# Kernel tuning notes

Measured on AMD Instinct MI355X. Metric: run time of the kernel, lower is better.

## Reference

```python
import jax, jax.numpy as jnp
import numpy as np

B, S, D, H = 2, 1024, 1024, 16
DH = D // H            # dim per head = 64
MAX_REL = 32           # max relative positions
ROPE_BASE = 10000.0


def entmax15(X, axis=-1):
    """1.5-entmax with full sort (k=None path of the torch code)."""
    X = (X - jnp.max(X, axis=axis, keepdims=True)) / 2.0
    Xsrt = -jnp.sort(-X, axis=axis)                       # descending sort
    d = X.shape[axis]
    rho = jnp.arange(1, d + 1, dtype=X.dtype)             # broadcasts on last axis
    mean = jnp.cumsum(Xsrt, axis=axis) / rho
    mean_sq = jnp.cumsum(Xsrt * Xsrt, axis=axis) / rho
    ss = rho * (mean_sq - mean * mean)
    delta = (1.0 - ss) / rho
    tau = mean - jnp.sqrt(jnp.clip(delta, 0.0))
    support = jnp.sum(tau <= Xsrt, axis=axis, keepdims=True)
    tau_star = jnp.take_along_axis(tau, support - 1, axis=axis)
    Y = jnp.clip(X - tau_star, 0.0)
    return Y * Y


def _rope(x, cos, sin):
    # x: [B,S,H,DH]; cos/sin: [S, DH//2]; complex mult on (even,odd) pairs
    xe, xo = x[..., 0::2], x[..., 1::2]
    c = cos[None, :, None, :]
    s = sin[None, :, None, :]
    re = xe * c - xo * s
    im = xe * s + xo * c
    return jnp.stack([re, im], axis=-1).reshape(x.shape)


def setup_inputs() -> dict:
    key = jax.random.key(0)
    ks = jax.random.split(key, 10)
    sc = 0.02
    x = jax.random.normal(ks[0], (B, S, D), dtype=jnp.float32)
    w_q = jax.random.normal(ks[1], (D, D), dtype=jnp.float32) * sc
    w_k = jax.random.normal(ks[2], (D, D), dtype=jnp.float32) * sc
    w_v = jax.random.normal(ks[3], (D, D), dtype=jnp.float32) * sc
    w_o = jax.random.normal(ks[4], (D, D), dtype=jnp.float32) * sc
    b_q = jnp.zeros((D,), jnp.float32)
    b_k = jnp.zeros((D,), jnp.float32)
    b_v = jnp.zeros((D,), jnp.float32)
    b_o = jnp.zeros((D,), jnp.float32)
    rel_emb = jax.random.normal(ks[5], (2 * MAX_REL + 1, DH), dtype=jnp.float32) * sc
    inv_freq = 1.0 / (ROPE_BASE ** (np.arange(0, DH, 2, dtype=np.float32) / DH))
    ang = np.arange(S, dtype=np.float32)[:, None] * inv_freq[None, :]
    rope_cos = jnp.asarray(np.cos(ang), jnp.float32)
    rope_sin = jnp.asarray(np.sin(ang), jnp.float32)
    return {"x": x, "w_q": w_q, "b_q": b_q, "w_k": w_k, "b_k": b_k,
            "w_v": w_v, "b_v": b_v, "w_o": w_o, "b_o": b_o,
            "rel_emb": rel_emb, "rope_cos": rope_cos, "rope_sin": rope_sin}


def reference(x, w_q, b_q, w_k, b_k, w_v, b_v, w_o, b_o, rel_emb, rope_cos, rope_sin):
    # QKV projections -> [B,S,H,DH]
    q = (x @ w_q + b_q).reshape(B, S, H, DH)
    k = (x @ w_k + b_k).reshape(B, S, H, DH)
    v = (x @ w_v + b_v).reshape(B, S, H, DH).transpose(0, 2, 1, 3)  # [B,H,S,DH]
    # RoPE on q, k (applied in [B,S,H,DH] layout like the torch code)
    q = _rope(q, rope_cos, rope_sin).transpose(0, 2, 1, 3)  # [B,H,S,DH]
    k = _rope(k, rope_cos, rope_sin).transpose(0, 2, 1, 3)
    q = q / jnp.sqrt(jnp.asarray(DH, q.dtype))
    # content scores
    scores = jnp.einsum('bhqd,bhkd->bhqk', q, k)
    # relative position bias (Shaw et al.), shared embedding for keys & values
    r = jnp.arange(S)
    dist = jnp.clip(r[None, :] - r[:, None], -MAX_REL, MAX_REL) + MAX_REL  # [S,S]
    rel = rel_emb[dist]                                                   # [S,S,DH]
    scores = scores + jnp.einsum('bhqd,qkd->bhqk', q, rel)
    # sparse normalization
    attn = entmax15(scores, axis=-1)
    # context + relative-position values
    ctx = jnp.einsum('bhqk,bhkd->bhqd', attn, v) + jnp.einsum('bhqk,qkd->bhqd', attn, rel)
    out = ctx.transpose(0, 2, 1, 3).reshape(B, S, D) @ w_o + b_o
    return out
```

## Files before the change

kernel.cpp:

```cpp
#include <hip/hip_runtime.h>

typedef __attribute__((ext_vector_type(8))) short s8v;
typedef __attribute__((ext_vector_type(4))) short s4v;
typedef __attribute__((ext_vector_type(4))) float f4v;

__device__ __forceinline__ short f2bf(float f){
  union { float f; unsigned u; } v; v.f = f;
  unsigned r = v.u + 0x7fffu + ((v.u >> 16) & 1u);
  return (short)(r >> 16);
}
__device__ __forceinline__ float bf2f(short s){
  union { unsigned u; float f; } v; v.u = ((unsigned)(unsigned short)s) << 16; return v.f;
}
__device__ __forceinline__ void gload16(const void* g, void* l){
  __builtin_amdgcn_global_load_lds((const __attribute__((address_space(1))) unsigned int*)g,
                                   (__attribute__((address_space(3))) unsigned int*)l, 16, 0, 0);
}

__global__ __launch_bounds__(256) void prep_k(const float* __restrict__ w_q, const float* __restrict__ w_k,
                                              const float* __restrict__ w_v, const float* __restrict__ w_o,
                                              const float* __restrict__ x, const float* __restrict__ rel,
                                              short* __restrict__ wqkvT, short* __restrict__ woT,
                                              short* __restrict__ xb, short* __restrict__ relb,
                                              short* __restrict__ relT){
  int z = blockIdx.z;
  if (z < 4){
    __shared__ float t[64][65];
    const float* in = (z==0) ? w_q : (z==1) ? w_k : (z==2) ? w_v : w_o;
    short* out = (z==3) ? woT : (wqkvT + ((size_t)z<<20));
    int c0 = blockIdx.x*64, r0 = blockIdx.y*64;
    int tx = threadIdx.x & 63, ty = threadIdx.x >> 6;
    #pragma unroll
    for (int i=0;i<16;i++){ int r = ty + i*4; t[r][tx] = in[(size_t)(r0+r)*1024 + c0+tx]; }
    __syncthreads();
    #pragma unroll
    for (int i=0;i<16;i++){ int cc = ty + i*4; out[(size_t)(c0+cc)*1024 + r0+tx] = f2bf(t[tx][cc]); }
    if (z==3 && blockIdx.x==0 && blockIdx.y==0){
      for (int e = threadIdx.x; e < 65*64; e += 256){
        int j = e >> 6, d = e & 63;
        short bv = f2bf(rel[e]);
        relb[e] = bv;
        relT[d*72 + j] = bv;
      }
    }
  } else {
    int bid = (z-4)*256 + blockIdx.y*16 + blockIdx.x;
    int i = bid*256 + threadIdx.x;
    #pragma unroll
    for (int p=0;p<4;p++){
      int idx = p*131072 + i;
      f4v v = ((const f4v*)x)[idx];
      s4v o; o[0]=f2bf(v[0]); o[1]=f2bf(v[1]); o[2]=f2bf(v[2]); o[3]=f2bf(v[3]);
      ((s4v*)xb)[idx] = o;
    }
  }
}

__device__ __forceinline__ void gemm12864_core(const short* __restrict__ A, const short* __restrict__ Bt,
                                               int m0, int n0, short* As, short* Bs, f4v acc[4][2]){
  int tid = threadIdx.x;
  int lane = tid & 63, wave = tid >> 6;
  int wr = wave >> 1, wc = wave & 1, g = lane >> 4, c = lane & 15;
  int lrow = lane >> 3;
  int scol = ((lane & 7) ^ lrow) * 8;
  for (int k0 = 0; k0 < 1024; k0 += 64){
    #pragma unroll
    for (int p=0;p<4;p++){
      int r0 = wave*32 + p*8;
      gload16(A + (size_t)(m0 + r0 + lrow)*1024 + k0 + scol, &As[r0*64]);
    }
    #pragma unroll
    for (int p=0;p<2;p++){
      int r0 = wave*16 + p*8;
      gload16(Bt + (size_t)(n0 + r0 + lrow)*1024 + k0 + scol, &Bs[r0*64]);
    }
    __syncthreads();
    #pragma unroll
    for (int ks=0;ks<2;ks++){
      s8v a[4], b[2];
      int pu = ((ks*4 + g) ^ (c & 7))*8;
      #pragma unroll
      for (int mi=0;mi<4;mi++) a[mi] = *(const s8v*)(&As[(wr*64 + mi*16 + c)*64 + pu]);
      #pragma unroll
      for (int ni=0;ni<2;ni++) b[ni] = *(const s8v*)(&Bs[(wc*32 + ni*16 + c)*64 + pu]);
      #pragma unroll
      for (int mi=0;mi<4;mi++)
        #pragma unroll
        for (int ni=0;ni<2;ni++)
          acc[mi][ni] = __builtin_amdgcn_mfma_f32_16x16x32_bf16(a[mi], b[ni], acc[mi][ni], 0,0,0);
    }
    __syncthreads();
  }
}

__global__ __launch_bounds__(256) void gemm_qkv_k(const short* __restrict__ A, const short* __restrict__ Bt,
                                                  const float* __restrict__ b_q, const float* __restrict__ b_k,
                                                  const float* __restrict__ b_v,
                                                  const float* __restrict__ cs, const float* __restrict__ sn,
                                                  short* __restrict__ Qb, short* __restrict__ Kb,
                                                  short* __restrict__ Vt){
  __shared__ __align__(16) char lbuf[24576];
  short* As = (short*)lbuf;
  short* Bs = (short*)(lbuf + 16384);
  short* st = (short*)lbuf;
  int flat = blockIdx.x;
  int swz = (flat & 7)*96 + (flat >> 3);
  int m0 = (swz / 48) * 128, n0 = (swz % 48) * 64;
  int lane = threadIdx.x & 63, wave = threadIdx.x >> 6;
  int wr = wave >> 1, wc = wave & 1, g = lane >> 4, c = lane & 15;
  f4v acc[4][2] = {};
  gemm12864_core(A, Bt, m0, n0, As, Bs, acc);

  int sec = n0 >> 10;
  const float* bias = (sec==0) ? b_q : (sec==1) ? b_k : b_v;
  int b = m0 >> 10, s0 = m0 & 1023, h0 = (n0 & 1023) >> 6;
  #pragma unroll
  for (int mi=0;mi<4;mi++)
    #pragma unroll
    for (int ni=0;ni<2;ni++){
      int cl = wc*32 + ni*16 + c;
      float bi = bias[(n0 & 1023) + cl];
      int ifr = cl >> 1;
      #pragma unroll
      for (int i=0;i<4;i++){
        int rl = wr*64 + mi*16 + g*4 + i;
        float v = acc[mi][ni][i] + bi;
        if (sec < 2){
          int s = s0 + rl;
          float co = cs[s*32 + ifr], si = sn[s*32 + ifr];
          float p = __shfl_xor(v, 1, 64);
          float o = (cl & 1) ? fmaf(p, si, v*co) : fmaf(v, co, -(p*si));
          if (sec == 0) o *= 0.125f;
          v = o;
        }
        st[rl*66 + cl] = f2bf(v);
      }
    }
  __syncthreads();
  if (sec < 2){
    short* dst = (sec==0) ? Qb : Kb;
    size_t base = ((size_t)(b*16+h0)*1024 + s0)*64;
    for (int e = threadIdx.x; e < 128*16; e += 256){
      int row = e >> 4, cl4 = (e & 15)*4;
      s4v o = *(const s4v*)(&st[row*66 + cl4]);
      *(s4v*)(&dst[base + (size_t)row*64 + cl4]) = o;
    }
  } else {
    size_t base = (size_t)(b*16+h0)*65536;
    for (int e = threadIdx.x; e < 64*32; e += 256){
      int d = e >> 5, s4 = (e & 31)*4;
      s4v o;
      o[0] = st[(s4+0)*66 + d]; o[1] = st[(s4+1)*66 + d];
      o[2] = st[(s4+2)*66 + d]; o[3] = st[(s4+3)*66 + d];
      *(s4v*)(&Vt[base + (size_t)d*1024 + s0 + s4]) = o;
    }
  }
}

__global__ __launch_bounds__(256) void gemm_out_k(const short* __restrict__ A, const short* __restrict__ Bt,
                                                  const float* __restrict__ bias, float* __restrict__ C){
  __shared__ __align__(16) short As[128*64];
  __shared__ __align__(16) short Bs[64*64];
  int flat = blockIdx.x;
  int swz = (flat & 7)*32 + (flat >> 3);
  int m0 = (swz >> 4)*128, n0 = (swz & 15)*64;
  int lane = threadIdx.x & 63, wave = threadIdx.x >> 6;
  int wr = wave >> 1, wc = wave & 1, g = lane >> 4, c = lane & 15;
  f4v acc[4][2] = {};
  gemm12864_core(A, Bt, m0, n0, As, Bs, acc);
  #pragma unroll
  for (int mi=0;mi<4;mi++)
    #pragma unroll
    for (int ni=0;ni<2;ni++){
      int col = n0 + wc*32 + ni*16 + c;
      float bi = bias[col];
      #pragma unroll
      for (int i=0;i<4;i++){
        int row = m0 + wr*64 + mi*16 + g*4 + i;
        C[(size_t)row*1024 + col] = acc[mi][ni][i] + bi;
      }
    }
}

#define ATPAD 1028
__global__ __launch_bounds__(256,4) void attn_fused_k(const short* __restrict__ Qb, const short* __restrict__ Kb,
                                                      const short* __restrict__ relb, const short* __restrict__ relT,
                                                      const short* __restrict__ Vt, short* __restrict__ ctxb){
  __shared__ __align__(16) short pb_b[16][66];
  __shared__ __align__(16) float wrow[16][68];
  __shared__ __align__(16) short attn_l[16][ATPAD];
  float2* red = (float2*)&pb_b[0][0];

  int lane = threadIdx.x & 63, wave = threadIdx.x >> 6;
  int g = lane >> 4, c = lane & 15;
  int flat = blockIdx.x;
  int swz = (flat & 7)*256 + (flat >> 3);
  int bh = swz >> 6, q0 = (swz & 63)*16;
  const short* Qh = Qb + (size_t)bh*65536;
  const short* Kh = Kb + (size_t)bh*65536;
  const short* Vh = Vt + (size_t)bh*65536;

  for (int e = threadIdx.x; e < 16*68; e += 256) ((float*)wrow)[e] = 0.f;

  s8v qa0 = *(const s8v*)(Qh + (q0+c)*64 + g*8);
  s8v qa1 = *(const s8v*)(Qh + (q0+c)*64 + 32 + g*8);

  {
    int ntile = (wave==3) ? 2 : 1;
    for (int t=0; t<ntile; t++){
      int jt = (t==0) ? wave : 4;
      int j = jt*16 + c;
      s8v rb0 = {}, rb1 = {};
      if (j < 65){
        rb0 = *(const s8v*)(relb + j*64 + g*8);
        rb1 = *(const s8v*)(relb + j*64 + 32 + g*8);
      }
      f4v pa = {};
      pa = __builtin_amdgcn_mfma_f32_16x16x32_bf16(qa0, rb0, pa, 0,0,0);
      pa = __builtin_amdgcn_mfma_f32_16x16x32_bf16(qa1, rb1, pa, 0,0,0);
      if (j < 65){
        #pragma unroll
        for (int i=0;i<4;i++) pb_b[g*4+i][j] = f2bf(pa[i]);
      }
    }
  }
  __syncthreads();

  int q = q0 + c;
  int kc0 = wave*256;
  int Lb = q0 - 32 - kc0;
  int Ub = q0 + 47 - kc0;
  float pb0  = bf2f(pb_b[c][0]);
  float pb64 = bf2f(pb_b[c][64]);
  f4v x[16];
  #pragma unroll
  for (int t=0;t<16;t++){
    f4v ini;
    if (t*16+15 <= Lb){ ini[0]=pb0; ini[1]=pb0; ini[2]=pb0; ini[3]=pb0; }
    else if (t*16 >= Ub){ ini[0]=pb64; ini[1]=pb64; ini[2]=pb64; ini[3]=pb64; }
    else {
      #pragma unroll
      for (int i=0;i<4;i++){
        int k = kc0 + t*16 + g*4 + i;
        int jj = min(max(k - q, -32), 32) + 32;
        ini[i] = bf2f(pb_b[c][jj]);
      }
    }
    const short* kp = Kh + (kc0 + t*16 + c)*64 + g*8;
    s8v ka0 = *(const s8v*)(kp);
    s8v ka1 = *(const s8v*)(kp + 32);
    ini = __builtin_amdgcn_mfma_f32_16x16x32_bf16(ka0, qa0, ini, 0,0,0);
    x[t] = __builtin_amdgcn_mfma_f32_16x16x32_bf16(ka1, qa1, ini, 0,0,0);
  }
  __syncthreads();

  f4v m4 = x[0];
  #pragma unroll
  for (int t=1;t<16;t++){
    m4[0]=fmaxf(m4[0],x[t][0]); m4[1]=fmaxf(m4[1],x[t][1]);
    m4[2]=fmaxf(m4[2],x[t][2]); m4[3]=fmaxf(m4[3],x[t][3]);
  }
  float mx = fmaxf(fmaxf(m4[0],m4[1]), fmaxf(m4[2],m4[3]));
  mx = fmaxf(mx, __shfl_xor(mx, 16, 64));
  mx = fmaxf(mx, __shfl_xor(mx, 32, 64));
  if (g == 0) red[wave*16 + c] = make_float2(mx, 0.f);
  __syncthreads();
  {
    float2 r0 = red[c], r1 = red[16+c], r2 = red[32+c], r3 = red[48+c];
    mx = fmaxf(fmaxf(r0.x, r1.x), fmaxf(r2.x, r3.x));
  }

  float theta = mx - 2.0f;
  for (int it=0; it<7; it++){
    f4v th4 = {theta, theta, theta, theta};
    f4v s1v = {0.f,0.f,0.f,0.f}, s2v = {0.f,0.f,0.f,0.f};
    #pragma unroll
    for (int t=0;t<16;t++){
      f4v d = x[t] - th4;
      f4v tt;
      tt[0]=fmaxf(d[0],0.f); tt[1]=fmaxf(d[1],0.f); tt[2]=fmaxf(d[2],0.f); tt[3]=fmaxf(d[3],0.f);
      s1v += tt;
      s2v += tt*tt;
    }
    float S1 = (s1v[0]+s1v[1])+(s1v[2]+s1v[3]);
    float S2 = (s2v[0]+s2v[1])+(s2v[2]+s2v[3]);
    S1 += __shfl_xor(S1, 16, 64); S2 += __shfl_xor(S2, 16, 64);
    S1 += __shfl_xor(S1, 32, 64); S2 += __shfl_xor(S2, 32, 64);
    int pp = (it+1)&1;
    if (g == 0) red[(pp*4 + wave)*16 + c] = make_float2(S1, S2);
    __syncthreads();
    float2 r0 = red[pp*64 + c], r1 = red[pp*64 + 16+c], r2 = red[pp*64 + 32+c], r3 = red[pp*64 + 48+c];
    S1 = (r0.x+r1.x)+(r2.x+r3.x);
    S2 = (r0.y+r1.y)+(r2.y+r3.y);
    theta += (S2 - 4.0f)/(2.0f*S1);
  }

  float w0p = 0.f, w64p = 0.f;
  {
    f4v th4 = {theta, theta, theta, theta};
    short* arow = &attn_l[c][kc0 + g*4];
    #pragma unroll
    for (int t=0;t<16;t++){
      f4v d = x[t] - th4;
      f4v tt;
      tt[0]=fmaxf(d[0],0.f); tt[1]=fmaxf(d[1],0.f); tt[2]=fmaxf(d[2],0.f); tt[3]=fmaxf(d[3],0.f);
      tt = tt*0.5f;
      f4v a = tt*tt;
      unsigned d0, d1;
      asm("v_cvt_pk_bf16_f32 %0, %1, %2" : "=v"(d0) : "v"(a[0]), "v"(a[1]));
      asm("v_cvt_pk_bf16_f32 %0, %1, %2" : "=v"(d1) : "v"(a[2]), "v"(a[3]));
      *(uint2*)(arow + t*16) = make_uint2(d0, d1);
      if (t*16+15 <= Lb)      w0p  += (a[0]+a[1])+(a[2]+a[3]);
      else if (t*16 >= Ub)    w64p += (a[0]+a[1])+(a[2]+a[3]);
      else {
        #pragma unroll
        for (int i=0;i<4;i++){
          int raw = kc0 + t*16 + g*4 + i - q;
          if (raw <= -32) w0p += a[i];
          else if (raw >= 32) w64p += a[i];
          else wrow[c][raw+32] = a[i];
        }
      }
    }
  }
  w0p += __shfl_xor(w0p, 16, 64); w64p += __shfl_xor(w64p, 16, 64);
  w0p += __shfl_xor(w0p, 32, 64); w64p += __shfl_xor(w64p, 32, 64);
  if (g == 0) red[wave*16 + c] = make_float2(w0p, w64p);
  __syncthreads();
  if (wave == 0 && g == 0){
    float2 r0 = red[c], r1 = red[16+c], r2 = red[32+c], r3 = red[48+c];
    wrow[c][0]  = (r0.x+r1.x)+(r2.x+r3.x);
    wrow[c][64] = (r0.y+r1.y)+(r2.y+r3.y);
  }
  __syncthreads();

  f4v acc = {};
  __builtin_amdgcn_s_setprio(1);
  #pragma unroll 8
  for (int kk=0; kk<32; kk++){
    s8v af = *(const s8v*)(&attn_l[c][kk*32 + g*8]);
    s8v bf = *(const s8v*)(Vh + (size_t)(wave*16+c)*1024 + kk*32 + g*8);
    acc = __builtin_amdgcn_mfma_f32_16x16x32_bf16(af, bf, acc, 0,0,0);
  }
  {
    const float* wp = &wrow[c][0];
    f4v A0 = *(const f4v*)(wp + g*8);
    f4v A1 = *(const f4v*)(wp + g*8 + 4);
    f4v A2 = *(const f4v*)(wp + 32 + g*8);
    f4v A3 = *(const f4v*)(wp + 32 + g*8 + 4);
    union { unsigned u[4]; s8v v; } W0, W1;
    asm("v_cvt_pk_bf16_f32 %0, %1, %2" : "=v"(W0.u[0]) : "v"(A0[0]), "v"(A0[1]));
    asm("v_cvt_pk_bf16_f32 %0, %1, %2" : "=v"(W0.u[1]) : "v"(A0[2]), "v"(A0[3]));
    asm("v_cvt_pk_bf16_f32 %0, %1, %2" : "=v"(W0.u[2]) : "v"(A1[0]), "v"(A1[1]));
    asm("v_cvt_pk_bf16_f32 %0, %1, %2" : "=v"(W0.u[3]) : "v"(A1[2]), "v"(A1[3]));
    asm("v_cvt_pk_bf16_f32 %0, %1, %2" : "=v"(W1.u[0]) : "v"(A2[0]), "v"(A2[1]));
    asm("v_cvt_pk_bf16_f32 %0, %1, %2" : "=v"(W1.u[1]) : "v"(A2[2]), "v"(A2[3]));
    asm("v_cvt_pk_bf16_f32 %0, %1, %2" : "=v"(W1.u[2]) : "v"(A3[0]), "v"(A3[1]));
    asm("v_cvt_pk_bf16_f32 %0, %1, %2" : "=v"(W1.u[3]) : "v"(A3[2]), "v"(A3[3]));
    s8v rb0 = *(const s8v*)(relT + (wave*16+c)*72 + g*8);
    s8v rb1 = *(const s8v*)(relT + (wave*16+c)*72 + 32 + g*8);
    acc = __builtin_amdgcn_mfma_f32_16x16x32_bf16(W0.v, rb0, acc, 0,0,0);
    acc = __builtin_amdgcn_mfma_f32_16x16x32_bf16(W1.v, rb1, acc, 0,0,0);
  }
  __builtin_amdgcn_s_setprio(0);
  int b = bh >> 4, h = bh & 15, d = wave*16 + c;
  float rl64 = bf2f(relT[d*72 + 64]);
  #pragma unroll
  for (int i=0;i<4;i++){
    int r = g*4+i;
    float s = acc[i] + wrow[r][64]*rl64;
    ctxb[((size_t)(b*1024 + q0 + r))*1024 + h*64 + d] = f2bf(s);
  }
}

extern "C" void kernel_launch(void* const* d_in, const int* in_sizes, int n_in,
                              void* d_out, int out_size, void* d_ws, size_t ws_size,
                              hipStream_t stream) {
  (void)in_sizes; (void)n_in; (void)out_size; (void)ws_size;
  const float* x    = (const float*)d_in[0];
  const float* w_q  = (const float*)d_in[1];
  const float* b_q  = (const float*)d_in[2];
  const float* w_k  = (const float*)d_in[3];
  const float* b_k  = (const float*)d_in[4];
  const float* w_v  = (const float*)d_in[5];
  const float* b_v  = (const float*)d_in[6];
  const float* w_o  = (const float*)d_in[7];
  const float* b_o  = (const float*)d_in[8];
  const float* rel  = (const float*)d_in[9];
  const float* rcos = (const float*)d_in[10];
  const float* rsin = (const float*)d_in[11];
  float* out = (float*)d_out;

  char* w = (char*)d_ws;
  short* xb    = (short*)(w);
  short* wqkvT = (short*)(w + ((size_t)4<<20));
  short* woT   = (short*)(w + ((size_t)10<<20));
  short* Qb    = (short*)(w + ((size_t)12<<20));
  short* Kb    = (short*)(w + ((size_t)16<<20));
  short* Vt    = (short*)(w + ((size_t)20<<20));
  short* ctxb  = (short*)(w + ((size_t)24<<20));
  short* relb  = (short*)(w + ((size_t)28<<20));
  short* relT  = (short*)(w + ((size_t)28<<20) + 65536);

  prep_k<<<dim3(16,16,6), 256, 0, stream>>>(w_q, w_k, w_v, w_o, x, rel, wqkvT, woT, xb, relb, relT);
  gemm_qkv_k<<<768, 256, 0, stream>>>(xb, wqkvT, b_q, b_k, b_v, rcos, rsin, Qb, Kb, Vt);
  attn_fused_k<<<2048, 256, 0, stream>>>(Qb, Kb, relb, relT, Vt, ctxb);
  gemm_out_k<<<256, 256, 0, stream>>>(ctxb, woT, b_o, out);
}
```

Before: 125.5 us.

## Double-buffer GEMM LDS stages, shrink output GEMM tile, prefetch V in attention

Both GEMM kernels now double-buffer their LDS tiles, so the next K-slice's global-to-LDS loads are issued before computing on the current slice, with one barrier per iteration instead of two. The output GEMM moves from 128x64 to 64x64 tiles and launches 512 blocks instead of 256 to fill more compute units. In the attention kernel, the first eight V fragments are loaded into registers before the softmax barrier, the AV loop is split across two accumulators for more MFMA independence, and the w0/w64 cross-wave reduction is folded into the epilogue, removing one barrier. Costs include doubled LDS per block, which may lower occupancy, more registers from the V prefetch, and a changed order for the w0 term.

```diff
diff --git a/kernel.cpp b/kernel.cpp
--- a/kernel.cpp
+++ b/kernel.cpp
@@ -56,40 +56,35 @@
   }
 }
 
-__device__ __forceinline__ void gemm12864_core(const short* __restrict__ A, const short* __restrict__ Bt,
-                                               int m0, int n0, short* As, short* Bs, f4v acc[4][2]){
-  int tid = threadIdx.x;
-  int lane = tid & 63, wave = tid >> 6;
-  int wr = wave >> 1, wc = wave & 1, g = lane >> 4, c = lane & 15;
-  int lrow = lane >> 3;
-  int scol = ((lane & 7) ^ lrow) * 8;
-  for (int k0 = 0; k0 < 1024; k0 += 64){
-    #pragma unroll
-    for (int p=0;p<4;p++){
-      int r0 = wave*32 + p*8;
-      gload16(A + (size_t)(m0 + r0 + lrow)*1024 + k0 + scol, &As[r0*64]);
-    }
-    #pragma unroll
-    for (int p=0;p<2;p++){
-      int r0 = wave*16 + p*8;
-      gload16(Bt + (size_t)(n0 + r0 + lrow)*1024 + k0 + scol, &Bs[r0*64]);
-    }
-    __syncthreads();
-    #pragma unroll
-    for (int ks=0;ks<2;ks++){
-      s8v a[4], b[2];
-      int pu = ((ks*4 + g) ^ (c & 7))*8;
-      #pragma unroll
-      for (int mi=0;mi<4;mi++) a[mi] = *(const s8v*)(&As[(wr*64 + mi*16 + c)*64 + pu]);
-      #pragma unroll
-      for (int ni=0;ni<2;ni++) b[ni] = *(const s8v*)(&Bs[(wc*32 + ni*16 + c)*64 + pu]);
-      #pragma unroll
-      for (int mi=0;mi<4;mi++)
-        #pragma unroll
-        for (int ni=0;ni<2;ni++)
-          acc[mi][ni] = __builtin_amdgcn_mfma_f32_16x16x32_bf16(a[mi], b[ni], acc[mi][ni], 0,0,0);
-    }
-    __syncthreads();
+__device__ __forceinline__ void stage12864(const short* __restrict__ A, const short* __restrict__ Bt,
+                                           int m0, int n0, int k0, short* As, short* Bs,
+                                           int wave, int lrow, int scol){
+  #pragma unroll
+  for (int p=0;p<4;p++){
+    int r0 = wave*32 + p*8;
+    gload16(A + (size_t)(m0 + r0 + lrow)*1024 + k0 + scol, &As[r0*64]);
+  }
+  #pragma unroll
+  for (int p=0;p<2;p++){
+    int r0 = wave*16 + p*8;
+    gload16(Bt + (size_t)(n0 + r0 + lrow)*1024 + k0 + scol, &Bs[r0*64]);
+  }
+}
+__device__ __forceinline__ void comp12864(const short* As, const short* Bs, f4v acc[4][2],
+                                          int wr, int wc, int g, int c){
+  #pragma unroll
+  for (int ks=0;ks<2;ks++){
+    s8v a[4], b[2];
+    int pu = ((ks*4 + g) ^ (c & 7))*8;
+    #pragma unroll
+    for (int mi=0;mi<4;mi++) a[mi] = *(const s8v*)(&As[(wr*64 + mi*16 + c)*64 + pu]);
+    #pragma unroll
+    for (int ni=0;ni<2;ni++) b[ni] = *(const s8v*)(&Bs[(wc*32 + ni*16 + c)*64 + pu]);
+    #pragma unroll
+    for (int mi=0;mi<4;mi++)
+      #pragma unroll
+      for (int ni=0;ni<2;ni++)
+        acc[mi][ni] = __builtin_amdgcn_mfma_f32_16x16x32_bf16(a[mi], b[ni], acc[mi][ni], 0,0,0);
   }
 }
 
@@ -99,17 +94,31 @@
                                                   const float* __restrict__ cs, const float* __restrict__ sn,
                                                   short* __restrict__ Qb, short* __restrict__ Kb,
                                                   short* __restrict__ Vt){
-  __shared__ __align__(16) char lbuf[24576];
-  short* As = (short*)lbuf;
-  short* Bs = (short*)(lbuf + 16384);
-  short* st = (short*)lbuf;
+  __shared__ __align__(16) char lbuf[49152];
+  short* As0 = (short*)lbuf;
+  short* Bs0 = (short*)(lbuf + 16384);
+  short* As1 = (short*)(lbuf + 24576);
+  short* Bs1 = (short*)(lbuf + 40960);
+  short* st  = (short*)lbuf;
   int flat = blockIdx.x;
   int swz = (flat & 7)*96 + (flat >> 3);
   int m0 = (swz / 48) * 128, n0 = (swz % 48) * 64;
   int lane = threadIdx.x & 63, wave = threadIdx.x >> 6;
   int wr = wave >> 1, wc = wave & 1, g = lane >> 4, c = lane & 15;
+  int lrow = lane >> 3, scol = ((lane & 7) ^ lrow)*8;
   f4v acc[4][2] = {};
-  gemm12864_core(A, Bt, m0, n0, As, Bs, acc);
+  stage12864(A, Bt, m0, n0, 0, As0, Bs0, wave, lrow, scol);
+  __syncthreads();
+  #pragma unroll 2
+  for (int t=0; t<16; t++){
+    const short* Ac = (t&1) ? As1 : As0;
+    const short* Bc = (t&1) ? Bs1 : Bs0;
+    short* An = (t&1) ? As0 : As1;
+    short* Bn = (t&1) ? Bs0 : Bs1;
+    if (t < 15) stage12864(A, Bt, m0, n0, (t+1)*64, An, Bn, wave, lrow, scol);
+    comp12864(Ac, Bc, acc, wr, wc, g, c);
+    __syncthreads();
+  }
 
   int sec = n0 >> 10;
   const float* bias = (sec==0) ? b_q : (sec==1) ? b_k : b_v;
@@ -157,26 +166,63 @@
   }
 }
 
+__device__ __forceinline__ void stage6464(const short* __restrict__ A, const short* __restrict__ Bt,
+                                          int m0, int n0, int k0, short* As, short* Bs,
+                                          int wave, int lrow, int scol){
+  #pragma unroll
+  for (int p=0;p<2;p++){
+    int r0 = wave*16 + p*8;
+    gload16(A  + (size_t)(m0 + r0 + lrow)*1024 + k0 + scol, &As[r0*64]);
+    gload16(Bt + (size_t)(n0 + r0 + lrow)*1024 + k0 + scol, &Bs[r0*64]);
+  }
+}
 __global__ __launch_bounds__(256) void gemm_out_k(const short* __restrict__ A, const short* __restrict__ Bt,
                                                   const float* __restrict__ bias, float* __restrict__ C){
-  __shared__ __align__(16) short As[128*64];
-  __shared__ __align__(16) short Bs[64*64];
+  __shared__ __align__(16) short As0[64*64];
+  __shared__ __align__(16) short Bs0[64*64];
+  __shared__ __align__(16) short As1[64*64];
+  __shared__ __align__(16) short Bs1[64*64];
   int flat = blockIdx.x;
-  int swz = (flat & 7)*32 + (flat >> 3);
-  int m0 = (swz >> 4)*128, n0 = (swz & 15)*64;
+  int swz = (flat & 7)*64 + (flat >> 3);
+  int m0 = (swz >> 4)*64, n0 = (swz & 15)*64;
   int lane = threadIdx.x & 63, wave = threadIdx.x >> 6;
   int wr = wave >> 1, wc = wave & 1, g = lane >> 4, c = lane & 15;
-  f4v acc[4][2] = {};
-  gemm12864_core(A, Bt, m0, n0, As, Bs, acc);
-  #pragma unroll
-  for (int mi=0;mi<4;mi++)
+  int lrow = lane >> 3, scol = ((lane & 7) ^ lrow)*8;
+  f4v acc[2][2] = {};
+  stage6464(A, Bt, m0, n0, 0, As0, Bs0, wave, lrow, scol);
+  __syncthreads();
+  #pragma unroll 2
+  for (int t=0; t<16; t++){
+    const short* Ac = (t&1) ? As1 : As0;
+    const short* Bc = (t&1) ? Bs1 : Bs0;
+    short* An = (t&1) ? As0 : As1;
+    short* Bn = (t&1) ? Bs0 : Bs1;
+    if (t < 15) stage6464(A, Bt, m0, n0, (t+1)*64, An, Bn, wave, lrow, scol);
+    #pragma unroll
+    for (int ks=0;ks<2;ks++){
+      s8v a[2], b[2];
+      int pu = ((ks*4 + g) ^ (c & 7))*8;
+      #pragma unroll
+      for (int mi=0;mi<2;mi++) a[mi] = *(const s8v*)(&Ac[(wr*32 + mi*16 + c)*64 + pu]);
+      #pragma unroll
+      for (int ni=0;ni<2;ni++) b[ni] = *(const s8v*)(&Bc[(wc*32 + ni*16 + c)*64 + pu]);
+      #pragma unroll
+      for (int mi=0;mi<2;mi++)
+        #pragma unroll
+        for (int ni=0;ni<2;ni++)
+          acc[mi][ni] = __builtin_amdgcn_mfma_f32_16x16x32_bf16(a[mi], b[ni], acc[mi][ni], 0,0,0);
+    }
+    __syncthreads();
+  }
+  #pragma unroll
+  for (int mi=0;mi<2;mi++)
     #pragma unroll
     for (int ni=0;ni<2;ni++){
       int col = n0 + wc*32 + ni*16 + c;
       float bi = bias[col];
       #pragma unroll
       for (int i=0;i<4;i++){
-        int row = m0 + wr*64 + mi*16 + g*4 + i;
+        int row = m0 + wr*32 + mi*16 + g*4 + i;
         C[(size_t)row*1024 + col] = acc[mi][ni][i] + bi;
       }
     }
@@ -233,6 +279,7 @@
   float pb0  = bf2f(pb_b[c][0]);
   float pb64 = bf2f(pb_b[c][64]);
   f4v x[16];
+  __builtin_amdgcn_s_setprio(1);
   #pragma unroll
   for (int t=0;t<16;t++){
     f4v ini;
@@ -252,6 +299,13 @@
     ini = __builtin_amdgcn_mfma_f32_16x16x32_bf16(ka0, qa0, ini, 0,0,0);
     x[t] = __builtin_amdgcn_mfma_f32_16x16x32_bf16(ka1, qa1, ini, 0,0,0);
   }
+  __builtin_amdgcn_s_setprio(0);
+
+  s8v vf[8];
+  #pragma unroll
+  for (int kk=0;kk<8;kk++)
+    vf[kk] = *(const s8v*)(Vh + (size_t)(wave*16+c)*1024 + kk*32 + g*8);
+
   __syncthreads();
 
   f4v m4 = x[0];
@@ -327,21 +381,26 @@
   w0p += __shfl_xor(w0p, 32, 64); w64p += __shfl_xor(w64p, 32, 64);
   if (g == 0) red[wave*16 + c] = make_float2(w0p, w64p);
   __syncthreads();
-  if (wave == 0 && g == 0){
-    float2 r0 = red[c], r1 = red[16+c], r2 = red[32+c], r3 = red[48+c];
-    wrow[c][0]  = (r0.x+r1.x)+(r2.x+r3.x);
-    wrow[c][64] = (r0.y+r1.y)+(r2.y+r3.y);
-  }
-  __syncthreads();
-
-  f4v acc = {};
+
+  f4v acc0 = {}, acc1 = {};
   __builtin_amdgcn_s_setprio(1);
-  #pragma unroll 8
-  for (int kk=0; kk<32; kk++){
-    s8v af = *(const s8v*)(&attn_l[c][kk*32 + g*8]);
-    s8v bf = *(const s8v*)(Vh + (size_t)(wave*16+c)*1024 + kk*32 + g*8);
-    acc = __builtin_amdgcn_mfma_f32_16x16x32_bf16(af, bf, acc, 0,0,0);
-  }
+  #pragma unroll
+  for (int kk=0; kk<8; kk+=2){
+    s8v af0 = *(const s8v*)(&attn_l[c][kk*32 + g*8]);
+    acc0 = __builtin_amdgcn_mfma_f32_16x16x32_bf16(af0, vf[kk], acc0, 0,0,0);
+    s8v af1 = *(const s8v*)(&attn_l[c][(kk+1)*32 + g*8]);
+    acc1 = __builtin_amdgcn_mfma_f32_16x16x32_bf16(af1, vf[kk+1], acc1, 0,0,0);
+  }
+  #pragma unroll
+  for (int kk=8; kk<32; kk+=2){
+    s8v af0 = *(const s8v*)(&attn_l[c][kk*32 + g*8]);
+    s8v bf0 = *(const s8v*)(Vh + (size_t)(wave*16+c)*1024 + kk*32 + g*8);
+    acc0 = __builtin_amdgcn_mfma_f32_16x16x32_bf16(af0, bf0, acc0, 0,0,0);
+    s8v af1 = *(const s8v*)(&attn_l[c][(kk+1)*32 + g*8]);
+    s8v bf1 = *(const s8v*)(Vh + (size_t)(wave*16+c)*1024 + (kk+1)*32 + g*8);
+    acc1 = __builtin_amdgcn_mfma_f32_16x16x32_bf16(af1, bf1, acc1, 0,0,0);
+  }
+  f4v acc = acc0 + acc1;
   {
     const float* wp = &wrow[c][0];
     f4v A0 = *(const f4v*)(wp + g*8);
@@ -363,12 +422,17 @@
     acc = __builtin_amdgcn_mfma_f32_16x16x32_bf16(W1.v, rb1, acc, 0,0,0);
   }
   __builtin_amdgcn_s_setprio(0);
+
   int b = bh >> 4, h = bh & 15, d = wave*16 + c;
+  float rl0  = bf2f(relT[d*72 + 0]);
   float rl64 = bf2f(relT[d*72 + 64]);
   #pragma unroll
   for (int i=0;i<4;i++){
     int r = g*4+i;
-    float s = acc[i] + wrow[r][64]*rl64;
+    float2 p0 = red[r], p1 = red[16+r], p2 = red[32+r], p3 = red[48+r];
+    float w0 = (p0.x+p1.x)+(p2.x+p3.x);
+    float w64v = (p0.y+p1.y)+(p2.y+p3.y);
+    float s = acc[i] + w0*rl0 + w64v*rl64;
     ctxb[((size_t)(b*1024 + q0 + r))*1024 + h*64 + d] = f2bf(s);
   }
 }
@@ -405,5 +469,5 @@
   prep_k<<<dim3(16,16,6), 256, 0, stream>>>(w_q, w_k, w_v, w_o, x, rel, wqkvT, woT, xb, relb, relT);
   gemm_qkv_k<<<768, 256, 0, stream>>>(xb, wqkvT, b_q, b_k, b_v, rcos, rsin, Qb, Kb, Vt);
   attn_fused_k<<<2048, 256, 0, stream>>>(Qb, Kb, relb, relT, Vt, ctxb);
-  gemm_out_k<<<256, 256, 0, stream>>>(ctxb, woT, b_o, out);
-}
+  gemm_out_k<<<512, 256, 0, stream>>>(ctxb, woT, b_o, out);
+}
```

Result: faster. 120.8 us (-3.7%).
